# Optimization experiments

Measured on AMD Instinct MI355X. Metric: run time of the kernel, lower is better.

The kernel has to match this reference:

```python
import jax, jax.numpy as jnp
import numpy as np

B, T, D = 16, 1024, 256   # batch, tokens, embedding_dim
Q, K = 4, 4096            # num_quantizers, n_embed
BETA = 1.0


def l2norm(x, eps=1e-12):
    n = jnp.linalg.norm(x, axis=-1, keepdims=True)
    return x / jnp.maximum(n, eps)


def vq_stage(z, codebook):
    """NormEMAVectorQuantizer forward (eval math; EMA buffer update omitted).
    z: (B,T,D) float; codebook: (K,D) l2-normalized rows.
    Returns straight-through quantized (B,T,D), scalar commit loss, indices (N,).
    """
    zn = l2norm(z)                                   # normalize input features
    zf = zn.reshape(-1, zn.shape[-1])                # (N, D)
    # squared euclidean distances (N, K): |z|^2 + |e|^2 - 2 z.e
    d = (jnp.sum(zf * zf, axis=1, keepdims=True)
         + jnp.sum(codebook * codebook, axis=1)[None, :]
         - 2.0 * zf @ codebook.T)
    idx = jnp.argmin(d, axis=1)                      # (N,)
    z_q = codebook[idx].reshape(zn.shape)            # gather codewords
    loss = BETA * jnp.mean((jax.lax.stop_gradient(z_q) - zn) ** 2)
    z_q = zn + jax.lax.stop_gradient(z_q - zn)       # straight-through
    return z_q, loss, idx


def setup_inputs() -> dict:
    key = jax.random.key(0)
    kx, kc = jax.random.split(key)
    x = jax.random.normal(kx, (B, T, D), dtype=jnp.float32)
    # EMA codebooks are kept l2-normalized in NormEMAVectorQuantizer
    codebooks = l2norm(jax.random.normal(kc, (Q, K, D), dtype=jnp.float32))
    return {"x": x, "codebooks": codebooks}


def reference(x, codebooks):
    residual = x
    quantized_outputs, losses, indices = [], [], []
    for q in range(codebooks.shape[0]):              # fixed small stage count
        z_q, loss, idx = vq_stage(residual, codebooks[q])
        # faithful to source: value of residual is unchanged, gradient path added
        residual = residual - jax.lax.stop_gradient(z_q) + z_q
        quantized_outputs.append(z_q)
        losses.append(loss)
        indices.append(idx)
    quantized_sum = quantized_outputs[0]
    for t in quantized_outputs[1:]:
        quantized_sum = quantized_sum + t
    total_loss = losses[0]
    for l in losses[1:]:
        total_loss = total_loss + l
    return quantized_sum, total_loss, jnp.stack(indices, axis=1)  # (N, Q) int
```

## Files before the change

kernel.cpp:

```cpp
#include <hip/hip_runtime.h>
#include <stdint.h>


#define NR 16384
#define DIM 256
#define KCB 4096
#define QST 4
#define MARGIN_DOT 4e-4f
#define MARGIN2_DOT 2e-5f
#define CAPL 4096

typedef _Float16 f16;
typedef __attribute__((ext_vector_type(4))) f16 f16x4;
typedef __attribute__((ext_vector_type(8))) f16 f16x8;
typedef __attribute__((ext_vector_type(4))) float f32x4;

#define WS_ZN_HI   ((size_t)0)
#define WS_ZN_LO   ((size_t)8*1024*1024)
#define WS_CB_HI   ((size_t)16*1024*1024)
#define WS_CB_LO   ((size_t)24*1024*1024)
#define WS_NORMS   ((size_t)32*1024*1024)
#define WS_SSQ     (WS_NORMS + 65536)
#define WS_TOPS    (WS_SSQ + 65536)
#define WS_IDX     (WS_TOPS + (size_t)QST*NR*2*16)
#define WS_LIST    (WS_IDX + (size_t)QST*NR*4)
#define WS_LIST2   (WS_LIST + (size_t)QST*CAPL*4)
#define WS_TOPS2   (WS_LIST2 + (size_t)QST*NR*4)
#define WS_CNT     (WS_TOPS2 + (size_t)QST*CAPL*8*16)
#define WS_PART    (WS_CNT + 64)
#define WS_TOPS3   (WS_PART + 16384)

__device__ __forceinline__ void gll16(const void* g, void* l) {
  __builtin_amdgcn_global_load_lds(
      (const __attribute__((address_space(1))) void*)g,
      (__attribute__((address_space(3))) void*)l, 16, 0, 0);
}

__device__ __forceinline__ float dot4chain(const float4* __restrict__ c,
                                           const float4* __restrict__ z) {
  float dot = 0.f;
  for (int d = 0; d < 64; ++d) {
    const float4 cv = c[d], zv = z[d];
    dot += cv.x * zv.x + cv.y * zv.y + cv.z * zv.z + cv.w * zv.w;
  }
  return dot;
}

__global__ void prep_kernel(const float* __restrict__ x, const float* __restrict__ cb,
                            char* __restrict__ ws) {
  const int w = threadIdx.x >> 6, lane = threadIdx.x & 63;
  const int normalize = (blockIdx.x < (NR / 4));
  const int blk = normalize ? blockIdx.x : blockIdx.x - (NR / 4);
  const float* src = normalize ? x : cb;
  const int row = blk * 4 + w;
  const float4 v = ((const float4*)src)[row * 64 + lane];
  float ss = v.x * v.x + v.y * v.y + v.z * v.z + v.w * v.w;
#pragma unroll
  for (int m = 32; m; m >>= 1) ss += __shfl_xor(ss, m);
  float4 z = v;
  f16 *hi, *lo;
  if (normalize) {
    const float denom = fmaxf(sqrtf(ss), 1e-12f);
    z.x = v.x / denom; z.y = v.y / denom; z.z = v.z / denom; z.w = v.w / denom;
    hi = (f16*)(ws + WS_ZN_HI); lo = (f16*)(ws + WS_ZN_LO);
    if (lane == 0) ((float*)(ws + WS_NORMS))[row] = denom;
    if (blockIdx.x == 0 && threadIdx.x < 8) ((int*)(ws + WS_CNT))[threadIdx.x] = 0;
  } else {
    hi = (f16*)(ws + WS_CB_HI); lo = (f16*)(ws + WS_CB_LO);
    if (lane == 0) ((float*)(ws + WS_SSQ))[row] = ss;
  }
  f16x4 h, l;
  h[0] = (f16)z.x; h[1] = (f16)z.y; h[2] = (f16)z.z; h[3] = (f16)z.w;
  l[0] = (f16)(z.x - (float)h[0]); l[1] = (f16)(z.y - (float)h[1]);
  l[2] = (f16)(z.z - (float)h[2]); l[3] = (f16)(z.w - (float)h[3]);
  ((f16x4*)hi)[row * 64 + lane] = h;
  ((f16x4*)lo)[row * 64 + lane] = l;
}

__launch_bounds__(256, 2)
__global__ void score_kernel(char* __restrict__ ws) {
  __shared__ __align__(16) f16 smem[2][2][128][64];
  const int tid = threadIdx.x, w = tid >> 6, lane = tid & 63;
  const int wr = w >> 1, wc = w & 1;
  const int blk = blockIdx.x;
  const int xcd = blk & 7, st = xcd >> 1;
  const int rowtile = ((xcd & 1) << 6) + (blk >> 3);
  const int rowBase = rowtile << 7;

  const f16* zn_hi = (const f16*)(ws + WS_ZN_HI);
  const f16* cb_hi = (const f16*)(ws + WS_CB_HI);

  const int reg = w >> 1;
  const int half = w & 1;
  const int g0 = (lane & 7) ^ ((lane >> 3) & 7);
  const size_t laneOff = (size_t)(lane >> 3) * DIM + (size_t)g0 * 8;
  const f16* srcA0 = zn_hi + (size_t)(rowBase + half * 64) * DIM + laneOff;
  const f16* srcB0 = cb_hi + ((size_t)st * KCB + half * 64) * DIM + laneOff;

  float t1[16], t2[16]; int i1[16];
#pragma unroll
  for (int s = 0; s < 16; ++s) { t1[s] = -3.4e38f; t2[s] = -3.4e38f; i1[s] = 0; }
  const int colLane = wc * 64 + (lane & 15);

  auto STAGE = [&](int b, int r) {
    const int ct = r >> 2, dc = r & 3;
    const f16* sp = reg ? (srcB0 + (size_t)ct * 128 * DIM + dc * 64)
                        : (srcA0 + dc * 64);
    f16* dst = &smem[b][reg][half * 64][0];
#pragma unroll
    for (int op = 0; op < 8; ++op)
      gll16(sp + op * 8 * DIM, dst + op * 512);
  };

  STAGE(0, 0);
  __syncthreads();

  f32x4 acc[4][4];
  const f32x4 zero4 = {0.f, 0.f, 0.f, 0.f};

  for (int r = 0; r < 128; ++r) {
    const int buf = r & 1;
    if (r + 1 < 128) STAGE(buf ^ 1, r + 1);
    const int dc = r & 3;
    const f16* As = &smem[buf][0][0][0];
    const f16* Bs = &smem[buf][1][0][0];
#pragma unroll
    for (int kk = 0; kk < 2; ++kk) {
      f16x8 ah[4];
#pragma unroll
      for (int m = 0; m < 4; ++m) {
        const int rl = wr * 64 + m * 16 + (lane & 15);
        const int slot = ((kk << 2) + (lane >> 4)) ^ (rl & 7);
        ah[m] = *(const f16x8*)(As + rl * 64 + slot * 8);
      }
#pragma unroll
      for (int n = 0; n < 4; ++n) {
        const int cl = wc * 64 + n * 16 + (lane & 15);
        const int slot = ((kk << 2) + (lane >> 4)) ^ (cl & 7);
        const f16x8 bh = *(const f16x8*)(Bs + cl * 64 + slot * 8);
        if (dc == 0 && kk == 0) {
#pragma unroll
          for (int m = 0; m < 4; ++m)
            acc[m][n] = __builtin_amdgcn_mfma_f32_16x16x32_f16(ah[m], bh, zero4, 0, 0, 0);
        } else {
#pragma unroll
          for (int m = 0; m < 4; ++m)
            acc[m][n] = __builtin_amdgcn_mfma_f32_16x16x32_f16(ah[m], bh, acc[m][n], 0, 0, 0);
        }
      }
    }
    if (dc == 3) {
      const int ct = r >> 2;
#pragma unroll
      for (int n = 0; n < 4; ++n) {
        const int col = ct * 128 + n * 16 + colLane;
#pragma unroll
        for (int m = 0; m < 4; ++m)
#pragma unroll
          for (int rr = 0; rr < 4; ++rr) {
            const float sc = acc[m][n][rr];
            const int sl = m * 4 + rr;
            if (sc > t1[sl]) { t2[sl] = t1[sl]; t1[sl] = sc; i1[sl] = col; }
            else t2[sl] = fmaxf(t2[sl], sc);
          }
      }
    }
    __syncthreads();
  }

  float* mv1 = (float*)&smem[0][0][0][0];
  float* mv2 = mv1 + 256;
  int*   mi1v = (int*)(mv2 + 256);
#pragma unroll
  for (int m = 0; m < 4; ++m)
#pragma unroll
    for (int rr = 0; rr < 4; ++rr) {
      const int sl = m * 4 + rr;
      float a1 = t1[sl], a2 = t2[sl]; int ai = i1[sl];
#pragma unroll
      for (int msk = 1; msk < 16; msk <<= 1) {
        const float o1 = __shfl_xor(a1, msk);
        const float o2 = __shfl_xor(a2, msk);
        const int   oi = __shfl_xor(ai, msk);
        if (o1 > a1)       { a2 = fmaxf(a1, o2); a1 = o1; ai = oi; }
        else if (o1 == a1) { a2 = a1; ai = min(ai, oi); }
        else               { a2 = fmaxf(a2, o1); }
      }
      if ((lane & 15) == 0) {
        const int rloc = wr * 64 + m * 16 + (lane >> 4) * 4 + rr;
        mv1[wc * 128 + rloc] = a1; mv2[wc * 128 + rloc] = a2; mi1v[wc * 128 + rloc] = ai;
      }
    }
  __syncthreads();
  if (tid < 128) {
    const float a1 = mv1[tid], a2 = mv2[tid]; const int ai = mi1v[tid];
    const float b1 = mv1[128 + tid], b2 = mv2[128 + tid]; const int bi = mi1v[128 + tid];
    float v1, v2; int fi;
    if (a1 > b1)      { v1 = a1; v2 = fmaxf(a2, b1); fi = ai; }
    else if (b1 > a1) { v1 = b1; v2 = fmaxf(b2, a1); fi = bi; }
    else { v1 = a1; v2 = a1; fi = min(ai, bi); }
    const int row = rowBase + tid;
    ((int*)(ws + WS_IDX))[row * 4 + st] = fi;
    if (v1 - v2 < MARGIN_DOT) {
      const int p = atomicAdd((int*)(ws + WS_CNT) + st, 1);
      if (p < CAPL) ((int*)(ws + WS_LIST))[st * CAPL + p] = row;
      else {
        const int p2 = atomicAdd((int*)(ws + WS_CNT) + 4 + st, 1);
        ((int*)(ws + WS_LIST2))[(size_t)st * NR + p2] = row;
      }
    }
  }
}

__launch_bounds__(256, 2)
__global__ void rescue_mfma_kernel(char* __restrict__ ws) {
  __shared__ __align__(16) f16 smem[4][128][64];
  __shared__ float mv1[2][128], mv2[2][128];
  __shared__ int   mi1[2][128];
  const int tid = threadIdx.x, w = tid >> 6, lane = tid & 63;
  const int wr = w >> 1, wc = w & 1;
  const int st = blockIdx.x & 3;
  const int kc = (blockIdx.x >> 2) & 7;
  const int slot = blockIdx.x >> 5;
  const int cnt = min(((const int*)(ws + WS_CNT))[st], CAPL);
  const int ntile = (cnt + 127) >> 7;
  const int* list = (const int*)(ws + WS_LIST) + st * CAPL;

  const f16* zn_hi = (const f16*)(ws + WS_ZN_HI);
  const f16* zn_lo = (const f16*)(ws + WS_ZN_LO);
  const f16* cb_hi = (const f16*)(ws + WS_CB_HI);
  const f16* cb_lo = (const f16*)(ws + WS_CB_LO);

  const int g0 = (lane & 7) ^ ((lane >> 3) & 7);
  const size_t laneOff = (size_t)(lane >> 3) * DIM + (size_t)g0 * 8;
  f16* ldsW = &smem[w][0][0];
  const f16* srcA = (w == 1) ? zn_lo : zn_hi;
  const f16* srcB = (w == 3) ? cb_lo : cb_hi;
  const int colLane = wc * 64 + (lane & 15);

  for (int tile = slot; tile < ntile; tile += 32) {
    const int base = tile << 7;
    int lid[16];
    if (w < 2) {
#pragma unroll
      for (int op = 0; op < 16; ++op) {
        const int i = base + op * 8 + (lane >> 3);
        lid[op] = list[min(i, cnt - 1)];
      }
    }
    float t1[16], t2[16]; int i1[16];
#pragma unroll
    for (int s = 0; s < 16; ++s) { t1[s] = -3.4e38f; t2[s] = -3.4e38f; i1[s] = 0; }

    for (int ct = kc * 4; ct < kc * 4 + 4; ++ct) {
      f32x4 acc[4][4];
#pragma unroll
      for (int m = 0; m < 4; ++m)
#pragma unroll
        for (int n = 0; n < 4; ++n) { acc[m][n][0] = 0.f; acc[m][n][1] = 0.f; acc[m][n][2] = 0.f; acc[m][n][3] = 0.f; }

      const f16* srcBBase = srcB + ((size_t)st * KCB + (size_t)ct * 128) * DIM + laneOff;

      for (int dc = 0; dc < 4; ++dc) {
        __syncthreads();
        if (w < 2) {
#pragma unroll
          for (int op = 0; op < 16; ++op)
            gll16(srcA + (size_t)lid[op] * DIM + dc * 64 + (size_t)g0 * 8,
                  ldsW + op * 512);
        } else {
          const f16* sp = srcBBase + dc * 64;
#pragma unroll
          for (int op = 0; op < 16; ++op)
            gll16(sp + op * 8 * DIM, ldsW + op * 512);
        }
        __syncthreads();

#pragma unroll
        for (int kk = 0; kk < 2; ++kk) {
          f16x8 ah[4], al[4];
#pragma unroll
          for (int m = 0; m < 4; ++m) {
            const int rl = wr * 64 + m * 16 + (lane & 15);
            const int slt = ((kk << 2) + (lane >> 4)) ^ (rl & 7);
            const int off = rl * 64 + slt * 8;
            ah[m] = *(const f16x8*)(&smem[0][0][0] + off);
            al[m] = *(const f16x8*)(&smem[1][0][0] + off);
          }
#pragma unroll
          for (int n = 0; n < 4; ++n) {
            const int cl = wc * 64 + n * 16 + (lane & 15);
            const int slt = ((kk << 2) + (lane >> 4)) ^ (cl & 7);
            const int off = cl * 64 + slt * 8;
            const f16x8 bh = *(const f16x8*)(&smem[2][0][0] + off);
            const f16x8 bl = *(const f16x8*)(&smem[3][0][0] + off);
#pragma unroll
            for (int m = 0; m < 4; ++m) {
              acc[m][n] = __builtin_amdgcn_mfma_f32_16x16x32_f16(ah[m], bh, acc[m][n], 0, 0, 0);
              acc[m][n] = __builtin_amdgcn_mfma_f32_16x16x32_f16(ah[m], bl, acc[m][n], 0, 0, 0);
              acc[m][n] = __builtin_amdgcn_mfma_f32_16x16x32_f16(al[m], bh, acc[m][n], 0, 0, 0);
            }
          }
        }
      }
#pragma unroll
      for (int n = 0; n < 4; ++n) {
        const int col = ct * 128 + n * 16 + colLane;
#pragma unroll
        for (int m = 0; m < 4; ++m)
#pragma unroll
          for (int r = 0; r < 4; ++r) {
            const float sc = acc[m][n][r];
            const int sl = m * 4 + r;
            if (sc > t1[sl]) { t2[sl] = t1[sl]; t1[sl] = sc; i1[sl] = col; }
            else t2[sl] = fmaxf(t2[sl], sc);
          }
      }
    }

#pragma unroll
    for (int m = 0; m < 4; ++m)
#pragma unroll
      for (int r = 0; r < 4; ++r) {
        const int sl = m * 4 + r;
        float a1 = t1[sl], a2 = t2[sl]; int ai = i1[sl];
#pragma unroll
        for (int msk = 1; msk < 16; msk <<= 1) {
          const float o1 = __shfl_xor(a1, msk);
          const float o2 = __shfl_xor(a2, msk);
          const int   oi = __shfl_xor(ai, msk);
          if (o1 > a1)       { a2 = fmaxf(a1, o2); a1 = o1; ai = oi; }
          else if (o1 == a1) { a2 = a1; ai = min(ai, oi); }
          else               { a2 = fmaxf(a2, o1); }
        }
        if ((lane & 15) == 0) {
          const int rloc = wr * 64 + m * 16 + (lane >> 4) * 4 + r;
          mv1[wc][rloc] = a1; mv2[wc][rloc] = a2; mi1[wc][rloc] = ai;
        }
      }
    __syncthreads();
    if (tid < 128 && base + tid < cnt) {
      const float a1 = mv1[0][tid], a2 = mv2[0][tid]; const int ai = mi1[0][tid];
      const float b1 = mv1[1][tid], b2 = mv2[1][tid]; const int bi = mi1[1][tid];
      float v1, v2; int fi;
      if (a1 > b1)      { v1 = a1; v2 = fmaxf(a2, b1); fi = ai; }
      else if (b1 > a1) { v1 = b1; v2 = fmaxf(b2, a1); fi = bi; }
      else { v1 = a1; v2 = a1; fi = min(ai, bi); }
      ((float4*)(ws + WS_TOPS2))[((size_t)(st * CAPL + base + tid) << 3) + kc] =
          make_float4(v1, v2, __int_as_float(fi), 0.f);
    }
    __syncthreads();
  }
}

__global__ void rescue_merge_kernel(char* __restrict__ ws) {
  const int t = blockIdx.x * 256 + threadIdx.x;
  const int st = t >> 12, j = t & (CAPL - 1);
  const int cnt = min(((const int*)(ws + WS_CNT))[st], CAPL);
  if (j >= cnt) return;
  const float4* p = (const float4*)(ws + WS_TOPS2) + ((size_t)(st * CAPL + j) << 3);
  float V1 = -3.4e38f, V2 = -3.4e38f; int I1 = 0;
#pragma unroll
  for (int c = 0; c < 8; ++c) {
    const float4 e = p[c];
    const float v1 = e.x, v2 = e.y; const int i1 = __float_as_int(e.z);
    if (v1 > V1) { V2 = fmaxf(V1, v2); V1 = v1; I1 = i1; }
    else {
      if (v1 == V1) I1 = min(I1, i1);
      V2 = fmaxf(V2, v1);
    }
  }
  const int row = ((const int*)(ws + WS_LIST))[st * CAPL + j];
  ((int*)(ws + WS_IDX))[row * 4 + st] = I1;
  if (V1 - V2 < MARGIN2_DOT) {
    const int p2 = atomicAdd((int*)(ws + WS_CNT) + 4 + st, 1);
    ((int*)(ws + WS_LIST2))[(size_t)st * NR + p2] = row;
  }
}

__global__ void rescue_exact_kernel(const float* __restrict__ x, const float* __restrict__ cb,
                                    char* __restrict__ ws) {
  __shared__ __align__(16) float zrow[DIM];
  __shared__ float zsq_s;
  __shared__ float lbv[4];
  __shared__ int   lbi[4];
  const int tid = threadIdx.x, w = tid >> 6, lane = tid & 63;
  const int st = blockIdx.x & 3;
  const int kc = (blockIdx.x >> 2) & 15;
  const int slot = blockIdx.x >> 6;
  const int cnt = min(((const int*)(ws + WS_CNT))[4 + st], CAPL);
  const int* list = (const int*)(ws + WS_LIST2) + (size_t)st * NR;
  const float* cbs = cb + (size_t)st * KCB * DIM;
  const float* ssqp = (const float*)(ws + WS_SSQ) + (size_t)st * KCB;
  int2* part = (int2*)(ws + WS_TOPS3);

  for (int j = slot; j < cnt; j += 16) {
    const int row = list[j];
    if (tid < 32) {
      const float denom = ((const float*)(ws + WS_NORMS))[row];
      const int g = tid;
      float ss = 0.f;
#pragma unroll
      for (int e = 0; e < 8; ++e) {
        const float v = x[(size_t)row * DIM + g * 8 + e] / denom;
        zrow[g * 8 + e] = v;
        ss += v * v;
      }
#pragma unroll
      for (int m = 16; m; m >>= 1) ss += __shfl_xor(ss, m);
      if (g == 0) zsq_s = ss;
    }
    __syncthreads();
    const float zsq = zsq_s;
    const int k = kc * 256 + tid;
    const float dot = dot4chain((const float4*)(cbs + (size_t)k * DIM), (const float4*)zrow);
    float bd = (zsq + ssqp[k]) - 2.0f * dot;
    int bi = k;
#pragma unroll
    for (int m = 32; m; m >>= 1) {
      const float od = __shfl_xor(bd, m);
      const int   oi = __shfl_xor(bi, m);
      if (od < bd || (od == bd && oi < bi)) { bd = od; bi = oi; }
    }
    if (lane == 0) { lbv[w] = bd; lbi[w] = bi; }
    __syncthreads();
    if (tid == 0) {
      float fb = lbv[0]; int fi = lbi[0];
#pragma unroll
      for (int ww = 1; ww < 4; ++ww)
        if (lbv[ww] < fb || (lbv[ww] == fb && lbi[ww] < fi)) { fb = lbv[ww]; fi = lbi[ww]; }
      part[((size_t)(st * CAPL + j) << 4) + kc] = make_int2(__float_as_int(fb), fi);
    }
    __syncthreads();
  }
}

__global__ void rescue_exact_merge_kernel(char* __restrict__ ws) {
  const int t = blockIdx.x * 256 + threadIdx.x;
  const int st = t >> 12, j = t & (CAPL - 1);
  const int cnt = min(((const int*)(ws + WS_CNT))[4 + st], CAPL);
  if (j >= cnt) return;
  const int2* part = (const int2*)(ws + WS_TOPS3) + ((size_t)(st * CAPL + j) << 4);
  float fb = 3.4e38f; int fi = 0x7fffffff;
#pragma unroll
  for (int kc = 0; kc < 16; ++kc) {
    const int2 e = part[kc];
    const float d = __int_as_float(e.x);
    if (d < fb || (d == fb && e.y < fi)) { fb = d; fi = e.y; }
  }
  const int row = ((const int*)(ws + WS_LIST2))[(size_t)st * NR + j];
  ((int*)(ws + WS_IDX))[row * 4 + st] = fi;
}

__global__ void rescue_tail_kernel(const float* __restrict__ x, const float* __restrict__ cb,
                                   char* __restrict__ ws) {
  __shared__ __align__(16) float zrows[8][DIM];
  __shared__ float zsqs[8];
  __shared__ float lbv[4][8];
  __shared__ int   lbi[4][8];
  const int tid = threadIdx.x, w = tid >> 6, lane = tid & 63;
  const int st = blockIdx.x & 3, slot = blockIdx.x >> 2;
  const int cnt = ((const int*)(ws + WS_CNT))[4 + st] - CAPL;
  if (cnt <= 0) return;
  const int nch = (cnt + 7) >> 3;
  const int* list = (const int*)(ws + WS_LIST2) + (size_t)st * NR + CAPL;
  const float* cbs = cb + (size_t)st * KCB * DIM;
  const float* ssqp = (const float*)(ws + WS_SSQ) + (size_t)st * KCB;

  for (int ch = slot; ch < nch; ch += 16) {
    const int base = ch * 8;
    const int nr = min(8, cnt - base);
    const int r = tid >> 5, g = tid & 31;
    if (r < nr) {
      const int row = list[base + r];
      const float denom = ((const float*)(ws + WS_NORMS))[row];
      float ss = 0.f;
#pragma unroll
      for (int j = 0; j < 8; ++j) {
        const float v = x[(size_t)row * DIM + g * 8 + j] / denom;
        zrows[r][g * 8 + j] = v;
        ss += v * v;
      }
#pragma unroll
      for (int m = 16; m; m >>= 1) ss += __shfl_xor(ss, m);
      if (g == 0) zsqs[r] = ss;
    }
    __syncthreads();

    float bd[8]; int bix[8];
#pragma unroll
    for (int q = 0; q < 8; ++q) { bd[q] = 3.4e38f; bix[q] = 0x7fffffff; }

    for (int k = tid; k < KCB; k += 256) {
      const float4* cr = (const float4*)(cbs + (size_t)k * DIM);
      const float4* zr = (const float4*)&zrows[0][0];
      float dot[8];
#pragma unroll
      for (int q = 0; q < 8; ++q) dot[q] = 0.f;
      for (int d = 0; d < 64; ++d) {
        const float4 cv = cr[d];
#pragma unroll
        for (int q = 0; q < 8; ++q) {
          const float4 zv = zr[q * 64 + d];
          dot[q] += cv.x * zv.x + cv.y * zv.y + cv.z * zv.z + cv.w * zv.w;
        }
      }
      const float sk = ssqp[k];
#pragma unroll
      for (int q = 0; q < 8; ++q) {
        const float dist = (zsqs[q] + sk) - 2.0f * dot[q];
        if (dist < bd[q]) { bd[q] = dist; bix[q] = k; }
      }
    }
#pragma unroll
    for (int q = 0; q < 8; ++q) {
#pragma unroll
      for (int m = 32; m; m >>= 1) {
        const float od = __shfl_xor(bd[q], m);
        const int   oi = __shfl_xor(bix[q], m);
        if (od < bd[q] || (od == bd[q] && oi < bix[q])) { bd[q] = od; bix[q] = oi; }
      }
      if (lane == 0) { lbv[w][q] = bd[q]; lbi[w][q] = bix[q]; }
    }
    __syncthreads();
    if (tid < 8 && tid < nr) {
      float fb = lbv[0][tid]; int fi = lbi[0][tid];
#pragma unroll
      for (int ww = 1; ww < 4; ++ww) {
        const float od = lbv[ww][tid]; const int oi = lbi[ww][tid];
        if (od < fb || (od == fb && oi < fi)) { fb = od; fi = oi; }
      }
      const int row = list[base + tid];
      ((int*)(ws + WS_IDX))[row * 4 + st] = fi;
    }
    __syncthreads();
  }
}

__global__ void finalize_kernel(const float* __restrict__ x, const float* __restrict__ cb,
                                char* __restrict__ ws, float* __restrict__ out) {
  __shared__ float wsum[4];
  const int w = threadIdx.x >> 6, lane = threadIdx.x & 63;
  const int row = blockIdx.x * 4 + w;
  const int* idxp = (const int*)(ws + WS_IDX) + (size_t)row * 4;
  const float denom = ((const float*)(ws + WS_NORMS))[row];
  const float4 xv = ((const float4*)x)[row * 64 + lane];
  const float4 zn = make_float4(xv.x / denom, xv.y / denom, xv.z / denom, xv.w / denom);
  float4 s = make_float4(0.f, 0.f, 0.f, 0.f);
  float lacc = 0.f;
#pragma unroll
  for (int q = 0; q < 4; ++q) {
    const int id = idxp[q];
    const float4 e = ((const float4*)(cb + ((size_t)q * KCB + id) * DIM))[lane];
    s.x += e.x; s.y += e.y; s.z += e.z; s.w += e.w;
    const float dx = e.x - zn.x, dy = e.y - zn.y, dz = e.z - zn.z, dw = e.w - zn.w;
    lacc += dx * dx + dy * dy + dz * dz + dw * dw;
  }
  ((float4*)out)[row * 64 + lane] = s;
  if (lane < 4) out[4194305 + (size_t)row * 4 + lane] = (float)idxp[lane];
#pragma unroll
  for (int m = 32; m; m >>= 1) lacc += __shfl_xor(lacc, m);
  if (lane == 0) wsum[w] = lacc;
  __syncthreads();
  if (threadIdx.x == 0)
    ((float*)(ws + WS_PART))[blockIdx.x] = wsum[0] + wsum[1] + wsum[2] + wsum[3];
}

__global__ void loss_final_kernel(const char* __restrict__ ws, float* __restrict__ out) {
  __shared__ float wsum[4];
  const int tid = threadIdx.x, w = tid >> 6, lane = tid & 63;
  const float* p = (const float*)(ws + WS_PART);
  float s = 0.f;
  for (int i = tid; i < 4096; i += 256) s += p[i];
#pragma unroll
  for (int m = 32; m; m >>= 1) s += __shfl_xor(s, m);
  if (lane == 0) wsum[w] = s;
  __syncthreads();
  if (tid == 0)
    out[4194304] = (wsum[0] + wsum[1] + wsum[2] + wsum[3]) * (1.0f / 4194304.0f);
}

extern "C" void kernel_launch(void* const* d_in, const int* in_sizes, int n_in,
                              void* d_out, int out_size, void* d_ws, size_t ws_size,
                              hipStream_t stream) {
  (void)in_sizes; (void)n_in; (void)out_size; (void)ws_size;
  const float* x = (const float*)d_in[0];
  const float* cb = (const float*)d_in[1];
  float* out = (float*)d_out;
  char* ws = (char*)d_ws;

  hipLaunchKernelGGL(prep_kernel, dim3(NR / 2), dim3(256), 0, stream, x, cb, ws);
  hipLaunchKernelGGL(score_kernel, dim3(512), dim3(256), 0, stream, ws);
  hipLaunchKernelGGL(rescue_mfma_kernel, dim3(1024), dim3(256), 0, stream, ws);
  hipLaunchKernelGGL(rescue_merge_kernel, dim3((QST * CAPL) / 256), dim3(256), 0, stream, ws);
  hipLaunchKernelGGL(rescue_exact_kernel, dim3(1024), dim3(256), 0, stream, x, cb, ws);
  hipLaunchKernelGGL(rescue_exact_merge_kernel, dim3((QST * CAPL) / 256), dim3(256), 0, stream, ws);
  hipLaunchKernelGGL(rescue_tail_kernel, dim3(64), dim3(256), 0, stream, x, cb, ws);
  hipLaunchKernelGGL(finalize_kernel, dim3(NR / 4), dim3(256), 0, stream, x, cb, ws, out);
  hipLaunchKernelGGL(loss_final_kernel, dim3(1), dim3(256), 0, stream, ws, out);
}
```

Measured before the change: 363.9 us.

## Unroll score loop by four phases and issue LDS reads before next-stage global loads

The double-buffered score GEMM loop is unrolled into four explicit phases per codebook tile, using separate named LDS buffers so buffer addresses and the dc==0/dc==3 conditions become compile-time constants. Within each phase all A/B fragments are read from LDS before the next tile's global-to-LDS loads are issued, and only then are the MFMAs run. The top-2 epilogue runs once per tile without a runtime branch. This removes per-iteration branching and indexing overhead and lets loads overlap the MFMAs, at the cost of more live registers for the fragment arrays, which may pressure the two-blocks-per-CU occupancy target.

```diff
diff --git a/kernel.cpp b/kernel.cpp
--- a/kernel.cpp
+++ b/kernel.cpp
@@ -79,7 +79,10 @@
 
 __launch_bounds__(256, 2)
 __global__ void score_kernel(char* __restrict__ ws) {
-  __shared__ __align__(16) f16 smem[2][2][128][64];
+  __shared__ __align__(16) f16 A0[128][64];
+  __shared__ __align__(16) f16 A1[128][64];
+  __shared__ __align__(16) f16 B0[128][64];
+  __shared__ __align__(16) f16 B1[128][64];
   const int tid = threadIdx.x, w = tid >> 6, lane = tid & 63;
   const int wr = w >> 1, wc = w & 1;
   const int blk = blockIdx.x;
@@ -97,78 +100,86 @@
   const f16* srcA0 = zn_hi + (size_t)(rowBase + half * 64) * DIM + laneOff;
   const f16* srcB0 = cb_hi + ((size_t)st * KCB + half * 64) * DIM + laneOff;
 
+  f16* dst0 = reg ? &B0[half * 64][0] : &A0[half * 64][0];
+  f16* dst1 = reg ? &B1[half * 64][0] : &A1[half * 64][0];
+
   float t1[16], t2[16]; int i1[16];
 #pragma unroll
   for (int s = 0; s < 16; ++s) { t1[s] = -3.4e38f; t2[s] = -3.4e38f; i1[s] = 0; }
   const int colLane = wc * 64 + (lane & 15);
 
-  auto STAGE = [&](int b, int r) {
-    const int ct = r >> 2, dc = r & 3;
-    const f16* sp = reg ? (srcB0 + (size_t)ct * 128 * DIM + dc * 64)
-                        : (srcA0 + dc * 64);
-    f16* dst = &smem[b][reg][half * 64][0];
+  auto SRC = [&](int ct, int dc) -> const f16* {
+    return reg ? (srcB0 + (size_t)ct * 128 * DIM + dc * 64) : (srcA0 + dc * 64);
+  };
+  auto STAGE = [&](f16* dst, const f16* sp) {
 #pragma unroll
     for (int op = 0; op < 8; ++op)
       gll16(sp + op * 8 * DIM, dst + op * 512);
   };
 
-  STAGE(0, 0);
-  __syncthreads();
-
   f32x4 acc[4][4];
   const f32x4 zero4 = {0.f, 0.f, 0.f, 0.f};
 
-  for (int r = 0; r < 128; ++r) {
-    const int buf = r & 1;
-    if (r + 1 < 128) STAGE(buf ^ 1, r + 1);
-    const int dc = r & 3;
-    const f16* As = &smem[buf][0][0][0];
-    const f16* Bs = &smem[buf][1][0][0];
+  auto PHASE = [&](const f16* As, const f16* Bs, f16* stDst, const f16* stSrc,
+                   bool doStage, bool init) {
+    f16x8 ah[2][4], bh[2][4];
 #pragma unroll
     for (int kk = 0; kk < 2; ++kk) {
-      f16x8 ah[4];
 #pragma unroll
       for (int m = 0; m < 4; ++m) {
         const int rl = wr * 64 + m * 16 + (lane & 15);
         const int slot = ((kk << 2) + (lane >> 4)) ^ (rl & 7);
-        ah[m] = *(const f16x8*)(As + rl * 64 + slot * 8);
+        ah[kk][m] = *(const f16x8*)(As + rl * 64 + slot * 8);
       }
 #pragma unroll
       for (int n = 0; n < 4; ++n) {
         const int cl = wc * 64 + n * 16 + (lane & 15);
         const int slot = ((kk << 2) + (lane >> 4)) ^ (cl & 7);
-        const f16x8 bh = *(const f16x8*)(Bs + cl * 64 + slot * 8);
-        if (dc == 0 && kk == 0) {
+        bh[kk][n] = *(const f16x8*)(Bs + cl * 64 + slot * 8);
+      }
+    }
+    if (doStage) STAGE(stDst, stSrc);
+#pragma unroll
+    for (int kk = 0; kk < 2; ++kk)
+#pragma unroll
+      for (int n = 0; n < 4; ++n) {
+        if (init && kk == 0) {
 #pragma unroll
           for (int m = 0; m < 4; ++m)
-            acc[m][n] = __builtin_amdgcn_mfma_f32_16x16x32_f16(ah[m], bh, zero4, 0, 0, 0);
+            acc[m][n] = __builtin_amdgcn_mfma_f32_16x16x32_f16(ah[0][m], bh[0][n], zero4, 0, 0, 0);
         } else {
 #pragma unroll
           for (int m = 0; m < 4; ++m)
-            acc[m][n] = __builtin_amdgcn_mfma_f32_16x16x32_f16(ah[m], bh, acc[m][n], 0, 0, 0);
+            acc[m][n] = __builtin_amdgcn_mfma_f32_16x16x32_f16(ah[kk][m], bh[kk][n], acc[m][n], 0, 0, 0);
         }
       }
-    }
-    if (dc == 3) {
-      const int ct = r >> 2;
-#pragma unroll
-      for (int n = 0; n < 4; ++n) {
-        const int col = ct * 128 + n * 16 + colLane;
-#pragma unroll
-        for (int m = 0; m < 4; ++m)
-#pragma unroll
-          for (int rr = 0; rr < 4; ++rr) {
-            const float sc = acc[m][n][rr];
-            const int sl = m * 4 + rr;
-            if (sc > t1[sl]) { t2[sl] = t1[sl]; t1[sl] = sc; i1[sl] = col; }
-            else t2[sl] = fmaxf(t2[sl], sc);
-          }
-      }
-    }
-    __syncthreads();
-  }
-
-  float* mv1 = (float*)&smem[0][0][0][0];
+    __syncthreads();
+  };
+
+  STAGE(dst0, SRC(0, 0));
+  __syncthreads();
+
+  for (int ct = 0; ct < 32; ++ct) {
+    PHASE(&A0[0][0], &B0[0][0], dst1, SRC(ct, 1), true, true);
+    PHASE(&A1[0][0], &B1[0][0], dst0, SRC(ct, 2), true, false);
+    PHASE(&A0[0][0], &B0[0][0], dst1, SRC(ct, 3), true, false);
+    PHASE(&A1[0][0], &B1[0][0], dst0, SRC(ct + 1, 0), ct < 31, false);
+#pragma unroll
+    for (int n = 0; n < 4; ++n) {
+      const int col = ct * 128 + n * 16 + colLane;
+#pragma unroll
+      for (int m = 0; m < 4; ++m)
+#pragma unroll
+        for (int rr = 0; rr < 4; ++rr) {
+          const float sc = acc[m][n][rr];
+          const int sl = m * 4 + rr;
+          if (sc > t1[sl]) { t2[sl] = t1[sl]; t1[sl] = sc; i1[sl] = col; }
+          else t2[sl] = fmaxf(t2[sl], sc);
+        }
+    }
+  }
+
+  float* mv1 = (float*)&A0[0][0];
   float* mv2 = mv1 + 256;
   int*   mi1v = (int*)(mv2 + 256);
 #pragma unroll
```

Result: faster. 350.2 us (-3.8%).
